# Performance work log

Hardware: AMD Instinct MI355X
Metric: run time of the kernel (lower is better)

Reference implementation:

```python
import jax, jax.numpy as jnp
import numpy as np


def setup_inputs() -> dict:
    key = jax.random.key(0)
    k1, k2, k3 = jax.random.split(key, 3)
    x = jax.random.normal(k1, (8, 2048, 512), dtype=jnp.float32)
    codebook = jax.random.normal(k2, (8192, 512), dtype=jnp.float32)
    values = jax.random.normal(k3, (8192, 512), dtype=jnp.float32)
    return {"x": x, "codebook": codebook, "values": values}


def reference(x, codebook, values):
    # VectorQuantize: nearest codebook entry under squared L2 distance.
    # dist(b,n,k) = ||x_bn||^2 - 2 x_bn . e_k + ||e_k||^2
    x_sq = jnp.sum(x * x, axis=-1, keepdims=True)            # [b, n, 1]
    e_sq = jnp.sum(codebook * codebook, axis=-1)             # [k]
    dots = jnp.einsum('bnd,kd->bnk', x, codebook)            # [b, n, k] (GEMM)
    memory_indices = jnp.argmin(x_sq - 2.0 * dots + e_sq, axis=-1)  # [b, n]
    # Irregular gather into the memory/value table.
    memories = values[memory_indices]                        # [b, n, dim_memory]
    return memories
```

## Files before the change

### kernel.cpp

```cpp
#include <hip/hip_runtime.h>
#include <hip/hip_bf16.h>


#define D      512
#define M      16384
#define NCODE  8192
#define KH     512
#define NSTEP  8
#define TILEG  131072

typedef float f32x4  __attribute__((ext_vector_type(4)));
typedef short bf16x8 __attribute__((ext_vector_type(8)));

#define KMAX 0xFFFFFFFFFFFFFFFFull

__device__ __forceinline__ void gload16(const __hip_bfloat16* g, __hip_bfloat16* l) {
  __builtin_amdgcn_global_load_lds(
      (const __attribute__((address_space(1))) void*)g,
      (__attribute__((address_space(3))) void*)l, 16, 0, 0);
}

__device__ __forceinline__ unsigned long long score_key(float sc, int code) {
  unsigned int u = __float_as_uint(sc);
  unsigned int su = u ^ ((unsigned int)((int)u >> 31) | 0x80000000u);
  return ((unsigned long long)su << 32) | (unsigned int)code;
}

__device__ __forceinline__ void kins2(unsigned long long k,
                                      unsigned long long& k1, unsigned long long& k2) {
  if (k < k1) { k2 = k1; k1 = k; }
  else if (k < k2) { k2 = k; }
}

__device__ __forceinline__ void kins4(unsigned long long k,
    unsigned long long& k0, unsigned long long& k1,
    unsigned long long& k2, unsigned long long& k3) {
  if (k < k0)      { k3 = k2; k2 = k1; k1 = k0; k0 = k; }
  else if (k < k1) { k3 = k2; k2 = k1; k1 = k; }
  else if (k < k2) { k3 = k2; k2 = k; }
  else if (k < k3) { k3 = k; }
}

__global__ __launch_bounds__(256)
void prep256(const float* __restrict__ src, __hip_bfloat16* __restrict__ dst) {
  __shared__ __hip_bfloat16 tile[256][72];
  const int tid = threadIdx.x;
  const int c = blockIdx.x & 7, t = blockIdx.x >> 3;
  const float* srow = src + (size_t)t * 256 * D;
  __hip_bfloat16* dbase = dst + (size_t)t * TILEG;

#pragma unroll
  for (int j = 0; j < 8; ++j) {
    int f = tid + j * 256;
    int row = f >> 3, k16l = f & 7;
    const float4* p = (const float4*)(srow + (size_t)row * D + c * 64 + k16l * 8);
    float4 v0 = p[0], v1 = p[1];
    float vv[8] = {v0.x, v0.y, v0.z, v0.w, v1.x, v1.y, v1.z, v1.w};
    union { bf16x8 v; unsigned short u[8]; } pk;
#pragma unroll
    for (int e = 0; e < 8; ++e) {
      __hip_bfloat16 h = __float2bfloat16(vv[e]);
      pk.u[e] = *(unsigned short*)&h;
    }
    *(bf16x8*)&tile[row][k16l * 8] = pk.v;
  }
  __syncthreads();
#pragma unroll
  for (int j = 0; j < 8; ++j) {
    int g = tid + j * 256;
    int row = g & 255, k16l = g >> 8;
    bf16x8 v = *(const bf16x8*)&tile[row][k16l * 8];
    *(bf16x8*)(dbase + ((size_t)(c * 8 + k16l) * 256 + row) * 8) = v;
  }
}

__global__ __launch_bounds__(256)
void rowsumsq(const float* __restrict__ src, float* __restrict__ dst, int nrows) {
  int gw = (blockIdx.x * 256 + threadIdx.x) >> 6;
  if (gw >= nrows) return;
  int lane = threadIdx.x & 63;
  const float4* s4 = (const float4*)(src + (size_t)gw * D);
  float s = 0.f;
#pragma unroll
  for (int i = 0; i < 2; ++i) {
    float4 v = s4[lane + i * 64];
    s += v.x * v.x + v.y * v.y + v.z * v.z + v.w * v.w;
  }
#pragma unroll
  for (int off = 32; off > 0; off >>= 1) s += __shfl_down(s, off, 64);
  if (lane == 0) dst[gw] = s;
}

__global__ __launch_bounds__(512, 1)
void vq_gemm256(const __hip_bfloat16* __restrict__ Apack,
                const __hip_bfloat16* __restrict__ Bpack,
                const float* __restrict__ e_sq,
                ulonglong2* __restrict__ cand2) {
  extern __shared__ __hip_bfloat16 smem[];

  const int tid = threadIdx.x;
  const int w = tid >> 6, l = tid & 63;
  const int wr = w >> 2, wc = w & 3;
  const int lr = l & 15, lh = l >> 4;

  const int bid = blockIdx.x;
  const int xcd = bid & 7, idx = bid >> 3;
  const int mt = xcd * 8 + (idx & 7);
  const int ct = idx >> 3;

  const __hip_bfloat16* Abase = Apack + (size_t)mt * TILEG;
  const __hip_bfloat16* Bbase = Bpack + (size_t)ct * TILEG;

  f32x4 acc[4][8] = {};

#define STAGE(buf, t)                                                           \
  do {                                                                          \
    _Pragma("unroll")                                                           \
    for (int i = 0; i < 4; ++i) {                                               \
      const int g = tid + i * 512;                                              \
      gload16(Abase + ((size_t)(t) * 2048 + g) * 8,                             \
              smem + ((size_t)(buf) * 4096 + g) * 8);                           \
      gload16(Bbase + ((size_t)(t) * 2048 + g) * 8,                             \
              smem + ((size_t)(buf) * 4096 + 2048 + g) * 8);                    \
    }                                                                           \
  } while (0)

#define COMPUTE(buf)                                                            \
  do {                                                                          \
    const bf16x8* Ag = (const bf16x8*)smem + (buf) * 4096;                      \
    const bf16x8* Bg = Ag + 2048;                                               \
    _Pragma("unroll")                                                           \
    for (int kk = 0; kk < 2; ++kk) {                                            \
      const int kb = (kk * 4 + lh) * 256;                                       \
      bf16x8 a[8], b[4];                                                        \
      _Pragma("unroll")                                                         \
      for (int nc = 0; nc < 4; ++nc) b[nc] = Bg[kb + wc * 64 + nc * 16 + lr];   \
      _Pragma("unroll")                                                         \
      for (int m = 0; m < 8; ++m)   a[m] = Ag[kb + wr * 128 + m * 16 + lr];     \
      _Pragma("unroll")                                                         \
      for (int nc = 0; nc < 4; ++nc)                                            \
        _Pragma("unroll")                                                       \
        for (int m = 0; m < 8; ++m)                                             \
          acc[nc][m] = __builtin_amdgcn_mfma_f32_16x16x32_bf16(b[nc], a[m],     \
                                                               acc[nc][m], 0, 0, 0); \
    }                                                                           \
  } while (0)

  STAGE(0, 0);
  __syncthreads();
#pragma unroll 1
  for (int t = 0; t < NSTEP - 1; ++t) {
    const int cur = t & 1;
    STAGE(cur ^ 1, t + 1);
    COMPUTE(cur);
    __syncthreads();
  }
  COMPUTE((NSTEP - 1) & 1);
#undef STAGE
#undef COMPUTE

  const int col0 = ct * 256 + wc * 64;
  float es[4][4];
#pragma unroll
  for (int nc = 0; nc < 4; ++nc) {
    float4 e4 = *(const float4*)&e_sq[col0 + nc * 16 + lh * 4];
    es[nc][0] = e4.x; es[nc][1] = e4.y; es[nc][2] = e4.z; es[nc][3] = e4.w;
  }
#pragma unroll
  for (int m = 0; m < 8; ++m) {
    unsigned long long k1 = KMAX, k2 = KMAX;
#pragma unroll
    for (int nc = 0; nc < 4; ++nc)
#pragma unroll
      for (int q = 0; q < 4; ++q) {
        int code = col0 + nc * 16 + lh * 4 + q;
        kins2(score_key(es[nc][q] - 2.0f * acc[nc][m][q], code), k1, k2);
      }
#pragma unroll
    for (int s = 16; s <= 32; s <<= 1) {
      unsigned long long o1 = __shfl_xor(k1, s, 64);
      unsigned long long o2 = __shfl_xor(k2, s, 64);
      kins2(o1, k1, k2);
      kins2(o2, k1, k2);
    }
    if (lh == 0) {
      int gRow = mt * 256 + wr * 128 + m * 16 + lr;
      cand2[(size_t)gRow * 128 + ct * 4 + wc] = make_ulonglong2(k1, k2);
    }
  }
}

__global__ __launch_bounds__(256)
void vq_merge4(const float* __restrict__ x, const float* __restrict__ cb,
               const float* __restrict__ values, const float* __restrict__ e_sq,
               const ulonglong2* __restrict__ cand2, float* __restrict__ out) {
  int row = blockIdx.x * 4 + (threadIdx.x >> 6);
  int l = threadIdx.x & 63;

  unsigned long long k0 = KMAX, k1 = KMAX, k2 = KMAX, k3 = KMAX;
  const ulonglong2* base = cand2 + (size_t)row * 128;
#pragma unroll
  for (int u = 0; u < 2; ++u) {
    ulonglong2 e = base[l + 64 * u];
    kins4(e.x, k0, k1, k2, k3);
    kins4(e.y, k0, k1, k2, k3);
  }
#pragma unroll
  for (int s = 1; s < 64; s <<= 1) {
    unsigned long long o0 = __shfl_xor(k0, s, 64), o1 = __shfl_xor(k1, s, 64);
    unsigned long long o2 = __shfl_xor(k2, s, 64), o3 = __shfl_xor(k3, s, 64);
    kins4(o0, k0, k1, k2, k3); kins4(o1, k0, k1, k2, k3);
    kins4(o2, k0, k1, k2, k3); kins4(o3, k0, k1, k2, k3);
  }
  int i0 = (int)(k0 & 8191), i1 = (int)(k1 & 8191);
  int i2 = (int)(k2 & 8191), i3 = (int)(k3 & 8191);

  const float4* xr = (const float4*)(x + (size_t)row * D);
  const float4* c0 = (const float4*)(cb + (size_t)i0 * D);
  const float4* c1 = (const float4*)(cb + (size_t)i1 * D);
  const float4* c2 = (const float4*)(cb + (size_t)i2 * D);
  const float4* c3 = (const float4*)(cb + (size_t)i3 * D);
  float xsq = 0.f, t0 = 0.f, t1 = 0.f, t2 = 0.f, t3 = 0.f;
#pragma unroll
  for (int u = 0; u < 2; ++u) {
    float4 xv = xr[l + 64 * u];
    float4 a = c0[l + 64 * u], b = c1[l + 64 * u];
    float4 c = c2[l + 64 * u], e = c3[l + 64 * u];
    xsq += xv.x * xv.x + xv.y * xv.y + xv.z * xv.z + xv.w * xv.w;
    t0 += xv.x * a.x + xv.y * a.y + xv.z * a.z + xv.w * a.w;
    t1 += xv.x * b.x + xv.y * b.y + xv.z * b.z + xv.w * b.w;
    t2 += xv.x * c.x + xv.y * c.y + xv.z * c.z + xv.w * c.w;
    t3 += xv.x * e.x + xv.y * e.y + xv.z * e.z + xv.w * e.w;
  }
#pragma unroll
  for (int s = 1; s < 64; s <<= 1) {
    xsq += __shfl_xor(xsq, s, 64);
    t0 += __shfl_xor(t0, s, 64); t1 += __shfl_xor(t1, s, 64);
    t2 += __shfl_xor(t2, s, 64); t3 += __shfl_xor(t3, s, 64);
  }
  float D0 = xsq - 2.0f * t0 + e_sq[i0];
  float D1 = xsq - 2.0f * t1 + e_sq[i1];
  float D2 = xsq - 2.0f * t2 + e_sq[i2];
  float D3 = xsq - 2.0f * t3 + e_sq[i3];
  float bdist = D0; int best = i0;
  if (D1 < bdist || (D1 == bdist && i1 < best)) { bdist = D1; best = i1; }
  if (D2 < bdist || (D2 == bdist && i2 < best)) { bdist = D2; best = i2; }
  if (D3 < bdist || (D3 == bdist && i3 < best)) { bdist = D3; best = i3; }

  const float4* vsrc = (const float4*)(values + (size_t)best * D);
  float4* dst = (float4*)(out + (size_t)row * D);
  dst[l] = vsrc[l];
  dst[l + 64] = vsrc[l + 64];
}

extern "C" void kernel_launch(void* const* d_in, const int* in_sizes, int n_in,
                              void* d_out, int out_size, void* d_ws, size_t ws_size,
                              hipStream_t stream) {
  const float* x      = (const float*)d_in[0];
  const float* cb     = (const float*)d_in[1];
  const float* values = (const float*)d_in[2];
  float* out = (float*)d_out;

  const size_t A_BYTES = (size_t)M * KH * 2;
  const size_t B_BYTES = (size_t)NCODE * KH * 2;
  const size_t C_BYTES = (size_t)M * 128 * 16;

  char* base = (char*)d_ws;
  __hip_bfloat16* Apack = (__hip_bfloat16*)base;
  __hip_bfloat16* Bpack = (__hip_bfloat16*)(base + A_BYTES);
  ulonglong2* cand2 = (ulonglong2*)(base + A_BYTES + B_BYTES);
  float* e_sq = (float*)(base + A_BYTES + B_BYTES + C_BYTES);

  const int LDS_GEMM = 131072;
  (void)hipFuncSetAttribute(reinterpret_cast<const void*>(vq_gemm256),
                            hipFuncAttributeMaxDynamicSharedMemorySize, LDS_GEMM);

  prep256<<<(M / 256) * 8, 256, 0, stream>>>(x, Apack);
  prep256<<<(NCODE / 256) * 8, 256, 0, stream>>>(cb, Bpack);
  rowsumsq<<<NCODE / 4, 256, 0, stream>>>(cb, e_sq, NCODE);
  vq_gemm256<<<(M / 256) * (NCODE / 256), 512, LDS_GEMM, stream>>>(
      Apack, Bpack, e_sq, cand2);
  vq_merge4<<<M / 4, 256, 0, stream>>>(x, cb, values, e_sq, cand2, out);
}
```

Measured before the change: 779.3 us.

## Shrink GEMM tile to 256x128 and stage via registers instead of direct LDS loads

The GEMM tile changes from 256x256 to 256x128 codes, with a new prep128 packing kernel for the codebook. Each wave's accumulator tile halves, which lowers register pressure, and the grid doubles to 1024 blocks. Direct global-to-LDS loads are replaced by loads into registers that are written to LDS after the MFMA compute, so the global latency overlaps with compute. In exchange, arithmetic intensity per block drops, A tiles are reloaded twice as often, and register staging adds VGPR use and extra LDS write instructions.

```diff
diff --git a/kernel.cpp b/kernel.cpp
--- a/kernel.cpp
+++ b/kernel.cpp
@@ -5,20 +5,14 @@
 #define D      512
 #define M      16384
 #define NCODE  8192
-#define KH     512
 #define NSTEP  8
-#define TILEG  131072
+#define ATILEG 131072
+#define BTILEG 65536
 
 typedef float f32x4  __attribute__((ext_vector_type(4)));
 typedef short bf16x8 __attribute__((ext_vector_type(8)));
 
 #define KMAX 0xFFFFFFFFFFFFFFFFull
-
-__device__ __forceinline__ void gload16(const __hip_bfloat16* g, __hip_bfloat16* l) {
-  __builtin_amdgcn_global_load_lds(
-      (const __attribute__((address_space(1))) void*)g,
-      (__attribute__((address_space(3))) void*)l, 16, 0, 0);
-}
 
 __device__ __forceinline__ unsigned long long score_key(float sc, int code) {
   unsigned int u = __float_as_uint(sc);
@@ -47,7 +41,7 @@
   const int tid = threadIdx.x;
   const int c = blockIdx.x & 7, t = blockIdx.x >> 3;
   const float* srow = src + (size_t)t * 256 * D;
-  __hip_bfloat16* dbase = dst + (size_t)t * TILEG;
+  __hip_bfloat16* dbase = dst + (size_t)t * ATILEG;
 
 #pragma unroll
   for (int j = 0; j < 8; ++j) {
@@ -75,6 +69,39 @@
 }
 
 __global__ __launch_bounds__(256)
+void prep128(const float* __restrict__ src, __hip_bfloat16* __restrict__ dst) {
+  __shared__ __hip_bfloat16 tile[128][72];
+  const int tid = threadIdx.x;
+  const int c = blockIdx.x & 7, t = blockIdx.x >> 3;
+  const float* srow = src + (size_t)t * 128 * D;
+  __hip_bfloat16* dbase = dst + (size_t)t * BTILEG;
+
+#pragma unroll
+  for (int j = 0; j < 4; ++j) {
+    int f = tid + j * 256;
+    int row = f >> 3, k16l = f & 7;
+    const float4* p = (const float4*)(srow + (size_t)row * D + c * 64 + k16l * 8);
+    float4 v0 = p[0], v1 = p[1];
+    float vv[8] = {v0.x, v0.y, v0.z, v0.w, v1.x, v1.y, v1.z, v1.w};
+    union { bf16x8 v; unsigned short u[8]; } pk;
+#pragma unroll
+    for (int e = 0; e < 8; ++e) {
+      __hip_bfloat16 h = __float2bfloat16(vv[e]);
+      pk.u[e] = *(unsigned short*)&h;
+    }
+    *(bf16x8*)&tile[row][k16l * 8] = pk.v;
+  }
+  __syncthreads();
+#pragma unroll
+  for (int j = 0; j < 4; ++j) {
+    int g = tid + j * 256;
+    int row = g & 127, k16l = g >> 7;
+    bf16x8 v = *(const bf16x8*)&tile[row][k16l * 8];
+    *(bf16x8*)(dbase + ((size_t)(c * 8 + k16l) * 128 + row) * 8) = v;
+  }
+}
+
+__global__ __launch_bounds__(256)
 void rowsumsq(const float* __restrict__ src, float* __restrict__ dst, int nrows) {
   int gw = (blockIdx.x * 256 + threadIdx.x) >> 6;
   if (gw >= nrows) return;
@@ -92,7 +119,7 @@
 }
 
 __global__ __launch_bounds__(512, 1)
-void vq_gemm256(const __hip_bfloat16* __restrict__ Apack,
+void vq_gemm_rs(const __hip_bfloat16* __restrict__ Apack,
                 const __hip_bfloat16* __restrict__ Bpack,
                 const float* __restrict__ e_sq,
                 ulonglong2* __restrict__ cand2) {
@@ -100,7 +127,7 @@
 
   const int tid = threadIdx.x;
   const int w = tid >> 6, l = tid & 63;
-  const int wr = w >> 2, wc = w & 3;
+  const int wr = w >> 1, wc = w & 1;
   const int lr = l & 15, lh = l >> 4;
 
   const int bid = blockIdx.x;
@@ -108,58 +135,70 @@
   const int mt = xcd * 8 + (idx & 7);
   const int ct = idx >> 3;
 
-  const __hip_bfloat16* Abase = Apack + (size_t)mt * TILEG;
-  const __hip_bfloat16* Bbase = Bpack + (size_t)ct * TILEG;
-
-  f32x4 acc[4][8] = {};
-
-#define STAGE(buf, t)                                                           \
-  do {                                                                          \
-    _Pragma("unroll")                                                           \
-    for (int i = 0; i < 4; ++i) {                                               \
-      const int g = tid + i * 512;                                              \
-      gload16(Abase + ((size_t)(t) * 2048 + g) * 8,                             \
-              smem + ((size_t)(buf) * 4096 + g) * 8);                           \
-      gload16(Bbase + ((size_t)(t) * 2048 + g) * 8,                             \
-              smem + ((size_t)(buf) * 4096 + 2048 + g) * 8);                    \
-    }                                                                           \
+  const __hip_bfloat16* Abase = Apack + (size_t)mt * ATILEG;
+  const __hip_bfloat16* Bbase = Bpack + (size_t)ct * BTILEG;
+
+  f32x4 acc[4][4] = {};
+  float4 rA[4], rB[2];
+
+#define LOADR(t)                                                               \
+  do {                                                                         \
+    _Pragma("unroll")                                                          \
+    for (int i = 0; i < 4; ++i)                                                \
+      rA[i] = *(const float4*)(Abase + ((size_t)(t) * 2048 + tid + i * 512) * 8); \
+    _Pragma("unroll")                                                          \
+    for (int i = 0; i < 2; ++i)                                                \
+      rB[i] = *(const float4*)(Bbase + ((size_t)(t) * 1024 + tid + i * 512) * 8); \
   } while (0)
 
-#define COMPUTE(buf)                                                            \
-  do {                                                                          \
-    const bf16x8* Ag = (const bf16x8*)smem + (buf) * 4096;                      \
-    const bf16x8* Bg = Ag + 2048;                                               \
-    _Pragma("unroll")                                                           \
-    for (int kk = 0; kk < 2; ++kk) {                                            \
-      const int kb = (kk * 4 + lh) * 256;                                       \
-      bf16x8 a[8], b[4];                                                        \
-      _Pragma("unroll")                                                         \
-      for (int nc = 0; nc < 4; ++nc) b[nc] = Bg[kb + wc * 64 + nc * 16 + lr];   \
-      _Pragma("unroll")                                                         \
-      for (int m = 0; m < 8; ++m)   a[m] = Ag[kb + wr * 128 + m * 16 + lr];     \
-      _Pragma("unroll")                                                         \
-      for (int nc = 0; nc < 4; ++nc)                                            \
-        _Pragma("unroll")                                                       \
-        for (int m = 0; m < 8; ++m)                                             \
-          acc[nc][m] = __builtin_amdgcn_mfma_f32_16x16x32_bf16(b[nc], a[m],     \
+#define WRITE(buf)                                                             \
+  do {                                                                         \
+    float4* Aw = (float4*)smem + (buf) * 3072;                                 \
+    float4* Bw = Aw + 2048;                                                    \
+    _Pragma("unroll")                                                          \
+    for (int i = 0; i < 4; ++i) Aw[tid + i * 512] = rA[i];                     \
+    _Pragma("unroll")                                                          \
+    for (int i = 0; i < 2; ++i) Bw[tid + i * 512] = rB[i];                     \
+  } while (0)
+
+#define COMPUTE(buf)                                                           \
+  do {                                                                         \
+    const bf16x8* Ag = (const bf16x8*)smem + (buf) * 3072;                     \
+    const bf16x8* Bg = Ag + 2048;                                              \
+    _Pragma("unroll")                                                          \
+    for (int kk = 0; kk < 2; ++kk) {                                           \
+      const int kb = kk * 4 + lh;                                              \
+      bf16x8 a[4], b[4];                                                       \
+      _Pragma("unroll")                                                        \
+      for (int nc = 0; nc < 4; ++nc) b[nc] = Bg[kb * 128 + wc * 64 + nc * 16 + lr]; \
+      _Pragma("unroll")                                                        \
+      for (int m = 0; m < 4; ++m)   a[m] = Ag[kb * 256 + wr * 64 + m * 16 + lr];    \
+      _Pragma("unroll")                                                        \
+      for (int nc = 0; nc < 4; ++nc)                                           \
+        _Pragma("unroll")                                                      \
+        for (int m = 0; m < 4; ++m)                                            \
+          acc[nc][m] = __builtin_amdgcn_mfma_f32_16x16x32_bf16(b[nc], a[m],    \
                                                                acc[nc][m], 0, 0, 0); \
-    }                                                                           \
+    }                                                                          \
   } while (0)
 
-  STAGE(0, 0);
+  LOADR(0);
+  WRITE(0);
   __syncthreads();
+
 #pragma unroll 1
   for (int t = 0; t < NSTEP - 1; ++t) {
-    const int cur = t & 1;
-    STAGE(cur ^ 1, t + 1);
-    COMPUTE(cur);
+    LOADR(t + 1);
+    COMPUTE(t & 1);
+    WRITE((t + 1) & 1);
     __syncthreads();
   }
   COMPUTE((NSTEP - 1) & 1);
-#undef STAGE
+#undef LOADR
+#undef WRITE
 #undef COMPUTE
 
-  const int col0 = ct * 256 + wc * 64;
+  const int col0 = ct * 128 + wc * 64;
   float es[4][4];
 #pragma unroll
   for (int nc = 0; nc < 4; ++nc) {
@@ -167,7 +206,7 @@
     es[nc][0] = e4.x; es[nc][1] = e4.y; es[nc][2] = e4.z; es[nc][3] = e4.w;
   }
 #pragma unroll
-  for (int m = 0; m < 8; ++m) {
+  for (int m = 0; m < 4; ++m) {
     unsigned long long k1 = KMAX, k2 = KMAX;
 #pragma unroll
     for (int nc = 0; nc < 4; ++nc)
@@ -184,8 +223,8 @@
       kins2(o2, k1, k2);
     }
     if (lh == 0) {
-      int gRow = mt * 256 + wr * 128 + m * 16 + lr;
-      cand2[(size_t)gRow * 128 + ct * 4 + wc] = make_ulonglong2(k1, k2);
+      int gRow = mt * 256 + wr * 64 + m * 16 + lr;
+      cand2[(size_t)gRow * 128 + ct * 2 + wc] = make_ulonglong2(k1, k2);
     }
   }
 }
@@ -261,8 +300,8 @@
   const float* values = (const float*)d_in[2];
   float* out = (float*)d_out;
 
-  const size_t A_BYTES = (size_t)M * KH * 2;
-  const size_t B_BYTES = (size_t)NCODE * KH * 2;
+  const size_t A_BYTES = (size_t)M * 512 * 2;
+  const size_t B_BYTES = (size_t)NCODE * 512 * 2;
   const size_t C_BYTES = (size_t)M * 128 * 16;
 
   char* base = (char*)d_ws;
@@ -271,14 +310,14 @@
   ulonglong2* cand2 = (ulonglong2*)(base + A_BYTES + B_BYTES);
   float* e_sq = (float*)(base + A_BYTES + B_BYTES + C_BYTES);
 
-  const int LDS_GEMM = 131072;
-  (void)hipFuncSetAttribute(reinterpret_cast<const void*>(vq_gemm256),
+  const int LDS_GEMM = 98304;
+  (void)hipFuncSetAttribute(reinterpret_cast<const void*>(vq_gemm_rs),
                             hipFuncAttributeMaxDynamicSharedMemorySize, LDS_GEMM);
 
   prep256<<<(M / 256) * 8, 256, 0, stream>>>(x, Apack);
-  prep256<<<(NCODE / 256) * 8, 256, 0, stream>>>(cb, Bpack);
+  prep128<<<(NCODE / 128) * 8, 256, 0, stream>>>(cb, Bpack);
   rowsumsq<<<NCODE / 4, 256, 0, stream>>>(cb, e_sq, NCODE);
-  vq_gemm256<<<(M / 256) * (NCODE / 256), 512, LDS_GEMM, stream>>>(
+  vq_gemm_rs<<<(M / 256) * (NCODE / 128), 512, LDS_GEMM, stream>>>(
       Apack, Bpack, e_sq, cand2);
   vq_merge4<<<M / 4, 256, 0, stream>>>(x, cb, values, e_sq, cand2, out);
 }
```

Result: slower. 815.8 us (+4.7%).

## Switch candidate GEMM from bf16 to per-row scaled int8 MFMA

Applied to the files above, without the earlier changes.

Adds a scales kernel that computes per-row absmax quantization scales and codebook squared norms, quantizes x and codebook to int8 in the packed tile layout, and runs the distance GEMM with int8 MFMA accumulating in int32. Scores are rescaled by the product of the row and code scales before the top-2 candidate selection, and the existing fp32 merge pass still picks the exact winner from those candidates. This halves operand bytes and LDS use and targets the higher int8 MFMA throughput. The cost is coarser quantization, which raises the risk that the true nearest code drops out of the top-2 candidates.

```diff
diff --git a/kernel.cpp b/kernel.cpp
--- a/kernel.cpp
+++ b/kernel.cpp
@@ -5,16 +5,15 @@
 #define D      512
 #define M      16384
 #define NCODE  8192
-#define KH     512
 #define NSTEP  8
-#define TILEG  131072
-
-typedef float f32x4  __attribute__((ext_vector_type(4)));
-typedef short bf16x8 __attribute__((ext_vector_type(8)));
+#define TILEB  131072
+
+typedef int  i32x4 __attribute__((ext_vector_type(4)));
+typedef float f32x4 __attribute__((ext_vector_type(4)));
 
 #define KMAX 0xFFFFFFFFFFFFFFFFull
 
-__device__ __forceinline__ void gload16(const __hip_bfloat16* g, __hip_bfloat16* l) {
+__device__ __forceinline__ void gload16(const void* g, void* l) {
   __builtin_amdgcn_global_load_lds(
       (const __attribute__((address_space(1))) void*)g,
       (__attribute__((address_space(3))) void*)l, 16, 0, 0);
@@ -42,61 +41,79 @@
 }
 
 __global__ __launch_bounds__(256)
-void prep256(const float* __restrict__ src, __hip_bfloat16* __restrict__ dst) {
-  __shared__ __hip_bfloat16 tile[256][72];
+void scales_kernel(const float* __restrict__ x, const float* __restrict__ cb,
+                   float* __restrict__ qmul_x, float* __restrict__ sval_x,
+                   float* __restrict__ qmul_e, float* __restrict__ sval_e,
+                   float* __restrict__ e_sq) {
+  int gw = (blockIdx.x * 256 + threadIdx.x) >> 6;
+  int lane = threadIdx.x & 63;
+  bool isx = gw < M;
+  int row = isx ? gw : gw - M;
+  const float4* s4 = (const float4*)((isx ? x : cb) + (size_t)row * D);
+  float ma = 0.f, ss = 0.f;
+#pragma unroll
+  for (int i = 0; i < 2; ++i) {
+    float4 v = s4[lane + i * 64];
+    ma = fmaxf(ma, fmaxf(fmaxf(fabsf(v.x), fabsf(v.y)), fmaxf(fabsf(v.z), fabsf(v.w))));
+    ss += v.x * v.x + v.y * v.y + v.z * v.z + v.w * v.w;
+  }
+#pragma unroll
+  for (int off = 32; off > 0; off >>= 1) {
+    ma = fmaxf(ma, __shfl_down(ma, off, 64));
+    ss += __shfl_down(ss, off, 64);
+  }
+  if (lane == 0) {
+    ma = fmaxf(ma, 1e-30f);
+    if (isx) { qmul_x[row] = 127.0f / ma; sval_x[row] = ma / 127.0f; }
+    else     { qmul_e[row] = 127.0f / ma; sval_e[row] = ma / 127.0f; e_sq[row] = ss; }
+  }
+}
+
+__global__ __launch_bounds__(256)
+void prep_i8(const float* __restrict__ src, const float* __restrict__ qmul,
+             char* __restrict__ dst) {
+  __shared__ char tile[256][80];
   const int tid = threadIdx.x;
   const int c = blockIdx.x & 7, t = blockIdx.x >> 3;
   const float* srow = src + (size_t)t * 256 * D;
-  __hip_bfloat16* dbase = dst + (size_t)t * TILEG;
-
-#pragma unroll
-  for (int j = 0; j < 8; ++j) {
+  char* dbase = dst + (size_t)t * TILEB;
+
+#pragma unroll
+  for (int j = 0; j < 4; ++j) {
     int f = tid + j * 256;
-    int row = f >> 3, k16l = f & 7;
-    const float4* p = (const float4*)(srow + (size_t)row * D + c * 64 + k16l * 8);
-    float4 v0 = p[0], v1 = p[1];
-    float vv[8] = {v0.x, v0.y, v0.z, v0.w, v1.x, v1.y, v1.z, v1.w};
-    union { bf16x8 v; unsigned short u[8]; } pk;
-#pragma unroll
-    for (int e = 0; e < 8; ++e) {
-      __hip_bfloat16 h = __float2bfloat16(vv[e]);
-      pk.u[e] = *(unsigned short*)&h;
+    int row = f >> 2, k16l = f & 3;
+    const float4* p = (const float4*)(srow + (size_t)row * D + c * 64 + k16l * 16);
+    float qm = qmul[t * 256 + row];
+    union { i32x4 v; signed char b[16]; } pk;
+#pragma unroll
+    for (int u = 0; u < 4; ++u) {
+      float4 v = p[u];
+      float vv[4] = {v.x, v.y, v.z, v.w};
+#pragma unroll
+      for (int e = 0; e < 4; ++e) {
+        int q = __float2int_rn(vv[e] * qm);
+        q = q > 127 ? 127 : (q < -127 ? -127 : q);
+        pk.b[u * 4 + e] = (signed char)q;
+      }
     }
-    *(bf16x8*)&tile[row][k16l * 8] = pk.v;
+    *(i32x4*)&tile[row][k16l * 16] = pk.v;
   }
   __syncthreads();
 #pragma unroll
-  for (int j = 0; j < 8; ++j) {
+  for (int j = 0; j < 4; ++j) {
     int g = tid + j * 256;
     int row = g & 255, k16l = g >> 8;
-    bf16x8 v = *(const bf16x8*)&tile[row][k16l * 8];
-    *(bf16x8*)(dbase + ((size_t)(c * 8 + k16l) * 256 + row) * 8) = v;
-  }
-}
-
-__global__ __launch_bounds__(256)
-void rowsumsq(const float* __restrict__ src, float* __restrict__ dst, int nrows) {
-  int gw = (blockIdx.x * 256 + threadIdx.x) >> 6;
-  if (gw >= nrows) return;
-  int lane = threadIdx.x & 63;
-  const float4* s4 = (const float4*)(src + (size_t)gw * D);
-  float s = 0.f;
-#pragma unroll
-  for (int i = 0; i < 2; ++i) {
-    float4 v = s4[lane + i * 64];
-    s += v.x * v.x + v.y * v.y + v.z * v.z + v.w * v.w;
-  }
-#pragma unroll
-  for (int off = 32; off > 0; off >>= 1) s += __shfl_down(s, off, 64);
-  if (lane == 0) dst[gw] = s;
+    i32x4 v = *(const i32x4*)&tile[row][k16l * 16];
+    *(i32x4*)(dbase + (((size_t)(c * 4 + k16l) * 256 + row) * 16)) = v;
+  }
 }
 
 __global__ __launch_bounds__(512, 1)
-void vq_gemm256(const __hip_bfloat16* __restrict__ Apack,
-                const __hip_bfloat16* __restrict__ Bpack,
+void vq_gemm_i8(const char* __restrict__ Apack, const char* __restrict__ Bpack,
                 const float* __restrict__ e_sq,
+                const float* __restrict__ sval_x, const float* __restrict__ sval_e,
                 ulonglong2* __restrict__ cand2) {
-  extern __shared__ __hip_bfloat16 smem[];
+  extern __shared__ char smem[];
 
   const int tid = threadIdx.x;
   const int w = tid >> 6, l = tid & 63;
@@ -108,42 +125,38 @@
   const int mt = xcd * 8 + (idx & 7);
   const int ct = idx >> 3;
 
-  const __hip_bfloat16* Abase = Apack + (size_t)mt * TILEG;
-  const __hip_bfloat16* Bbase = Bpack + (size_t)ct * TILEG;
-
-  f32x4 acc[4][8] = {};
-
-#define STAGE(buf, t)                                                           \
-  do {                                                                          \
-    _Pragma("unroll")                                                           \
-    for (int i = 0; i < 4; ++i) {                                               \
-      const int g = tid + i * 512;                                              \
-      gload16(Abase + ((size_t)(t) * 2048 + g) * 8,                             \
-              smem + ((size_t)(buf) * 4096 + g) * 8);                           \
-      gload16(Bbase + ((size_t)(t) * 2048 + g) * 8,                             \
-              smem + ((size_t)(buf) * 4096 + 2048 + g) * 8);                    \
-    }                                                                           \
+  const char* Abase = Apack + (size_t)mt * TILEB;
+  const char* Bbase = Bpack + (size_t)ct * TILEB;
+
+  i32x4 acc[4][8] = {};
+
+#define STAGE(buf, t)                                                          \
+  do {                                                                         \
+    _Pragma("unroll")                                                          \
+    for (int i = 0; i < 2; ++i) {                                              \
+      const int g = tid + i * 512;                                             \
+      gload16(Abase + ((size_t)(t) * 1024 + g) * 16,                           \
+              smem + ((size_t)(buf) * 2048 + g) * 16);                         \
+      gload16(Bbase + ((size_t)(t) * 1024 + g) * 16,                           \
+              smem + ((size_t)(buf) * 2048 + 1024 + g) * 16);                  \
+    }                                                                          \
   } while (0)
 
-#define COMPUTE(buf)                                                            \
-  do {                                                                          \
-    const bf16x8* Ag = (const bf16x8*)smem + (buf) * 4096;                      \
-    const bf16x8* Bg = Ag + 2048;                                               \
-    _Pragma("unroll")                                                           \
-    for (int kk = 0; kk < 2; ++kk) {                                            \
-      const int kb = (kk * 4 + lh) * 256;                                       \
-      bf16x8 a[8], b[4];                                                        \
-      _Pragma("unroll")                                                         \
-      for (int nc = 0; nc < 4; ++nc) b[nc] = Bg[kb + wc * 64 + nc * 16 + lr];   \
-      _Pragma("unroll")                                                         \
-      for (int m = 0; m < 8; ++m)   a[m] = Ag[kb + wr * 128 + m * 16 + lr];     \
-      _Pragma("unroll")                                                         \
-      for (int nc = 0; nc < 4; ++nc)                                            \
-        _Pragma("unroll")                                                       \
-        for (int m = 0; m < 8; ++m)                                             \
-          acc[nc][m] = __builtin_amdgcn_mfma_f32_16x16x32_bf16(b[nc], a[m],     \
-                                                               acc[nc][m], 0, 0, 0); \
-    }                                                                           \
+#define COMPUTE(buf)                                                           \
+  do {                                                                         \
+    const i32x4* Ag = (const i32x4*)smem + (buf) * 2048;                       \
+    const i32x4* Bg = Ag + 1024;                                               \
+    i32x4 a[8], b[4];                                                          \
+    _Pragma("unroll")                                                          \
+    for (int nc = 0; nc < 4; ++nc) b[nc] = Bg[lh * 256 + wc * 64 + nc * 16 + lr]; \
+    _Pragma("unroll")                                                          \
+    for (int m = 0; m < 8; ++m)   a[m] = Ag[lh * 256 + wr * 128 + m * 16 + lr];   \
+    _Pragma("unroll")                                                          \
+    for (int nc = 0; nc < 4; ++nc)                                             \
+      _Pragma("unroll")                                                        \
+      for (int m = 0; m < 8; ++m)                                              \
+        acc[nc][m] = __builtin_amdgcn_mfma_i32_16x16x64_i8(b[nc], a[m],        \
+                                                           acc[nc][m], 0, 0, 0); \
   } while (0)
 
   STAGE(0, 0);
@@ -160,21 +173,29 @@
 #undef COMPUTE
 
   const int col0 = ct * 256 + wc * 64;
-  float es[4][4];
+  float es[4][4], sev[4][4], sxv[8];
 #pragma unroll
   for (int nc = 0; nc < 4; ++nc) {
     float4 e4 = *(const float4*)&e_sq[col0 + nc * 16 + lh * 4];
+    float4 s4 = *(const float4*)&sval_e[col0 + nc * 16 + lh * 4];
     es[nc][0] = e4.x; es[nc][1] = e4.y; es[nc][2] = e4.z; es[nc][3] = e4.w;
-  }
+    sev[nc][0] = s4.x; sev[nc][1] = s4.y; sev[nc][2] = s4.z; sev[nc][3] = s4.w;
+  }
+#pragma unroll
+  for (int m = 0; m < 8; ++m)
+    sxv[m] = sval_x[mt * 256 + wr * 128 + m * 16 + lr];
+
 #pragma unroll
   for (int m = 0; m < 8; ++m) {
     unsigned long long k1 = KMAX, k2 = KMAX;
+    const float sx2 = 2.0f * sxv[m];
 #pragma unroll
     for (int nc = 0; nc < 4; ++nc)
 #pragma unroll
       for (int q = 0; q < 4; ++q) {
         int code = col0 + nc * 16 + lh * 4 + q;
-        kins2(score_key(es[nc][q] - 2.0f * acc[nc][m][q], code), k1, k2);
+        float sc = es[nc][q] - sx2 * sev[nc][q] * (float)acc[nc][m][q];
+        kins2(score_key(sc, code), k1, k2);
       }
 #pragma unroll
     for (int s = 16; s <= 32; s <<= 1) {
@@ -261,24 +282,29 @@
   const float* values = (const float*)d_in[2];
   float* out = (float*)d_out;
 
-  const size_t A_BYTES = (size_t)M * KH * 2;
-  const size_t B_BYTES = (size_t)NCODE * KH * 2;
+  const size_t A_BYTES = (size_t)M * D;
+  const size_t B_BYTES = (size_t)NCODE * D;
   const size_t C_BYTES = (size_t)M * 128 * 16;
 
   char* base = (char*)d_ws;
-  __hip_bfloat16* Apack = (__hip_bfloat16*)base;
-  __hip_bfloat16* Bpack = (__hip_bfloat16*)(base + A_BYTES);
+  char* Apack = base;
+  char* Bpack = base + A_BYTES;
   ulonglong2* cand2 = (ulonglong2*)(base + A_BYTES + B_BYTES);
-  float* e_sq = (float*)(base + A_BYTES + B_BYTES + C_BYTES);
-
-  const int LDS_GEMM = 131072;
-  (void)hipFuncSetAttribute(reinterpret_cast<const void*>(vq_gemm256),
+  float* qmul_x = (float*)(base + A_BYTES + B_BYTES + C_BYTES);
+  float* sval_x = qmul_x + M;
+  float* qmul_e = sval_x + M;
+  float* sval_e = qmul_e + NCODE;
+  float* e_sq   = sval_e + NCODE;
+
+  const int LDS_GEMM = 65536;
+  (void)hipFuncSetAttribute(reinterpret_cast<const void*>(vq_gemm_i8),
                             hipFuncAttributeMaxDynamicSharedMemorySize, LDS_GEMM);
 
-  prep256<<<(M / 256) * 8, 256, 0, stream>>>(x, Apack);
-  prep256<<<(NCODE / 256) * 8, 256, 0, stream>>>(cb, Bpack);
-  rowsumsq<<<NCODE / 4, 256, 0, stream>>>(cb, e_sq, NCODE);
-  vq_gemm256<<<(M / 256) * (NCODE / 256), 512, LDS_GEMM, stream>>>(
-      Apack, Bpack, e_sq, cand2);
+  scales_kernel<<<(M + NCODE) / 4, 256, 0, stream>>>(
+      x, cb, qmul_x, sval_x, qmul_e, sval_e, e_sq);
+  prep_i8<<<(M / 256) * 8, 256, 0, stream>>>(x, qmul_x, Apack);
+  prep_i8<<<(NCODE / 256) * 8, 256, 0, stream>>>(cb, qmul_e, Bpack);
+  vq_gemm_i8<<<(M / 256) * (NCODE / 256), 512, LDS_GEMM, stream>>>(
+      Apack, Bpack, e_sq, sval_x, sval_e, cand2);
   vq_merge4<<<M / 4, 256, 0, stream>>>(x, cb, values, e_sq, cand2, out);
 }
```

Result: faster. 740.0 us (-5.0%).
